# Kernel optimization log

Measured on AMD Instinct MI355X. Metric: run time of the kernel, lower is better.

The kernel has to match this reference:

```python
import jax, jax.numpy as jnp
import numpy as np

N = 50000      # nodes
E = 800000     # edges
GENE = 64      # gene_dim
HID = 128      # hidden_dim
NCLS = 10      # num_classes
EPS = 1e-5


def setup_inputs() -> dict:
    key = jax.random.key(0)
    ks = jax.random.split(key, 4)
    inp = {
        "x": jax.random.normal(ks[0], (N, GENE), jnp.float32),
        "edge_index": jax.random.randint(ks[1], (2, E), 0, N),
    }
    # PNA-style conv: concat([x, 4 aggregators x 3 scalers]) -> 13*d_in features
    dims = [(GENE, HID), (HID, 2 * HID), (2 * HID, HID), (HID, HID // 2)]
    for i, (din, dout) in enumerate(dims, 1):
        k = jax.random.fold_in(key, i)
        inp[f"W{i}"] = jax.random.normal(k, (13 * din, dout), jnp.float32) / float(np.sqrt(13 * din))
        inp[f"b{i}"] = jnp.zeros((dout,), jnp.float32)
        inp[f"gamma{i}"] = jnp.ones((dout,), jnp.float32)
        inp[f"beta{i}"] = jnp.zeros((dout,), jnp.float32)
    inp["Wc"] = jax.random.normal(ks[2], (HID // 2, NCLS), jnp.float32) / float(np.sqrt(HID // 2))
    inp["bc"] = jnp.zeros((NCLS,), jnp.float32)
    return inp


def _pna(x, src, dst, deg, log_deg, delta, W, b):
    # gather source features along edges: [E, d]
    msg = x[src]
    cnt = jnp.maximum(deg, 1.0)[:, None]
    s = jax.ops.segment_sum(msg, dst, num_segments=N)
    mean = s / cnt
    mean_sq = jax.ops.segment_sum(msg * msg, dst, num_segments=N) / cnt
    std = jnp.sqrt(jnp.maximum(mean_sq - mean * mean, 0.0) + EPS)
    has = (deg > 0)[:, None]
    mn = jnp.where(has, jax.ops.segment_min(msg, dst, num_segments=N), 0.0)
    mx = jnp.where(has, jax.ops.segment_max(msg, dst, num_segments=N), 0.0)
    aggs = jnp.concatenate([mean, mn, mx, std], axis=-1)  # [N, 4d]
    amp = (log_deg / delta)[:, None]                       # amplification scaler
    att = jnp.where(log_deg > 0, delta / jnp.maximum(log_deg, 1e-6), 1.0)[:, None]
    feat = jnp.concatenate([x, aggs, aggs * amp, aggs * att], axis=-1)  # [N, 13d]
    return feat @ W + b


def _bn(h, gamma, beta):
    m = h.mean(axis=0)
    v = h.var(axis=0)
    return (h - m) / jnp.sqrt(v + EPS) * gamma + beta


def reference(x, edge_index, W1, b1, gamma1, beta1, W2, b2, gamma2, beta2,
              W3, b3, gamma3, beta3, W4, b4, gamma4, beta4, Wc, bc):
    src, dst = edge_index[0], edge_index[1]
    deg = jax.ops.segment_sum(jnp.ones((E,), jnp.float32), dst, num_segments=N)
    log_deg = jnp.log1p(deg)
    delta = log_deg.mean()
    h = _pna(x, src, dst, deg, log_deg, delta, W1, b1)
    h = _bn(jax.nn.relu(h), gamma1, beta1)
    h = _pna(h, src, dst, deg, log_deg, delta, W2, b2)
    h = _bn(jax.nn.relu(h), gamma2, beta2)
    h = _pna(h, src, dst, deg, log_deg, delta, W3, b3)
    h = _bn(jax.nn.relu(h), gamma3, beta3)
    h = _pna(h, src, dst, deg, log_deg, delta, W4, b4)
    h = _bn(jax.nn.relu(h), gamma4, beta4)
    return h @ Wc + bc
```

## Files before the change

### kernel.cpp

```cpp
#include <hip/hip_runtime.h>
#include <hip/hip_bf16.h>

#define NN 50000
#define NE 800000
#define EPSV 1e-5f
#define NB 49

typedef _Float16 h8 __attribute__((ext_vector_type(8)));
typedef _Float16 h4 __attribute__((ext_vector_type(4)));
typedef float    f4 __attribute__((ext_vector_type(4)));


__global__ void k_deg(const int* __restrict__ dst, int* __restrict__ deg){
  int e = blockIdx.x*blockDim.x + threadIdx.x;
  if(e < NE) atomicAdd(&deg[dst[e]], 1);
}

__global__ void k_logdeg(const int* __restrict__ deg, float* __restrict__ logdeg,
                         float* __restrict__ dsum){
  int i = blockIdx.x*blockDim.x + threadIdx.x;
  float v = 0.f;
  if(i < NN){ v = log1pf((float)deg[i]); logdeg[i] = v; }
  __shared__ float sh[256];
  sh[threadIdx.x] = v; __syncthreads();
  for(int off=128; off>0; off>>=1){
    if(threadIdx.x < off) sh[threadIdx.x] += sh[threadIdx.x+off];
    __syncthreads();
  }
  if(threadIdx.x == 0) atomicAdd(dsum, sh[0]);
}

__global__ void k_scalers(const float* __restrict__ logdeg, const float* __restrict__ dsum,
                          float* __restrict__ amp, float* __restrict__ att){
  int i = blockIdx.x*blockDim.x + threadIdx.x;
  if(i >= NN) return;
  float delta = dsum[0] / (float)NN;
  float ld = logdeg[i];
  amp[i] = ld / delta;
  att[i] = (ld > 0.f) ? (delta / fmaxf(ld, 1e-6f)) : 1.f;
}

__global__ void k_scan1(const int* __restrict__ deg, int* __restrict__ rowptr,
                        int* __restrict__ bsum){
  __shared__ int buf[1024];
  int tid = threadIdx.x;
  int i = blockIdx.x*1024 + tid;
  int v = (i < NN) ? deg[i] : 0;
  buf[tid] = v; __syncthreads();
  for(int off=1; off<1024; off<<=1){
    int t = (tid >= off) ? buf[tid-off] : 0;
    __syncthreads();
    buf[tid] += t;
    __syncthreads();
  }
  if(i < NN) rowptr[i] = buf[tid] - v;
  if(tid == 1023) bsum[blockIdx.x] = buf[1023];
}

__global__ void k_scan2(int* __restrict__ bsum){
  if(threadIdx.x == 0){
    int s = 0;
    for(int b = 0; b < NB; b++){ int t = bsum[b]; bsum[b] = s; s += t; }
    bsum[NB] = s;
  }
}

__global__ void k_scan3(int* __restrict__ rowptr, int* __restrict__ cursor,
                        const int* __restrict__ bsum){
  int i = blockIdx.x*256 + threadIdx.x;
  if(i < NN){
    int v = rowptr[i] + bsum[i >> 10];
    rowptr[i] = v; cursor[i] = v;
  }
  if(i == NN) rowptr[NN] = bsum[NB];
}

__global__ void k_fill(const int* __restrict__ src, const int* __restrict__ dst,
                       int* __restrict__ cursor, int* __restrict__ colidx){
  int e = blockIdx.x*blockDim.x + threadIdx.x;
  if(e < NE){
    int pos = atomicAdd(&cursor[dst[e]], 1);
    colidx[pos] = src[e];
  }
}

__global__ void k_cvtx(const float* __restrict__ x, _Float16* __restrict__ act){
  int i = blockIdx.x*256 + threadIdx.x;
  if(i < NN*64) act[i] = (_Float16)x[i];
}

__global__ void k_coef_id(float* __restrict__ cs, float* __restrict__ csh,
                          _Float16* __restrict__ cs16, _Float16* __restrict__ csh16){
  int c = threadIdx.x;
  cs[c] = 1.f; csh[c] = 0.f;
  cs16[c] = (_Float16)1.f; csh16[c] = (_Float16)0.f;
}

__global__ void k_bn_coef(const float* __restrict__ colsum, const float* __restrict__ colss,
                          const float* __restrict__ gamma, const float* __restrict__ beta,
                          int dout, float* __restrict__ cs, float* __restrict__ csh,
                          _Float16* __restrict__ cs16, _Float16* __restrict__ csh16){
  int c = threadIdx.x;
  if(c >= dout) return;
  float mean = colsum[c] / (float)NN;
  float var  = colss[c] / (float)NN - mean*mean;
  float inv  = rsqrtf(fmaxf(var, 0.f) + EPSV);
  float a = inv * gamma[c];
  float b = beta[c] - mean * a;
  cs[c] = a; csh[c] = b;
  cs16[c] = (_Float16)a; csh16[c] = (_Float16)b;
}


__global__ __launch_bounds__(256) void k_agg8(
    const _Float16* __restrict__ act, int d,
    const int* __restrict__ rowptr, const int* __restrict__ colidx,
    const float* __restrict__ cs, const float* __restrict__ csh,
    _Float16* __restrict__ aggs, size_t aggN)
{
  int wv = threadIdx.x >> 6, lane = threadIdx.x & 63;
  int lpn = d >> 3;
  int npw = 64 / lpn;
  int n = blockIdx.x*(npw*4) + wv*npw + (lane / lpn);
  int c = (lane % lpn) * 8;
  if(n >= NN) return;
  int beg = rowptr[n], end = rowptr[n+1];
  const _Float16* hp = act + c;

  float s[8], q[8], mn[8], mx[8];
  #pragma unroll
  for(int j = 0; j < 8; j++){ s[j]=0.f; q[j]=0.f; mn[j]=INFINITY; mx[j]=-INFINITY; }

#define ACC8(v) { _Pragma("unroll") for(int j=0;j<8;j++){ float a=(float)(v)[j]; \
    s[j]+=a; q[j]+=a*a; mn[j]=fminf(mn[j],a); mx[j]=fmaxf(mx[j],a); } }

  int e = beg;
  for(; e+4 <= end; e+=4){
    int i0=colidx[e], i1=colidx[e+1], i2=colidx[e+2], i3=colidx[e+3];
    h8 v0 = *(const h8*)(hp + (size_t)i0*d);
    h8 v1 = *(const h8*)(hp + (size_t)i1*d);
    h8 v2 = *(const h8*)(hp + (size_t)i2*d);
    h8 v3 = *(const h8*)(hp + (size_t)i3*d);
    ACC8(v0) ACC8(v1) ACC8(v2) ACC8(v3)
  }
  for(; e < end; e++){
    h8 v = *(const h8*)(hp + (size_t)colidx[e]*d);
    ACC8(v)
  }
#undef ACC8

  float cnt = (end>beg) ? (float)(end-beg) : 1.f;
  h8 vm, vn, vx, vs;
  #pragma unroll
  for(int j = 0; j < 8; j++){
    float a = cs[c+j], b = csh[c+j];
    float mean_r = s[j]/cnt;
    float var_r  = fmaxf(q[j]/cnt - mean_r*mean_r, 0.f);
    float meanp = a*mean_r + b;
    float mnp = (a >= 0.f) ? a*mn[j]+b : a*mx[j]+b;
    float mxp = (a >= 0.f) ? a*mx[j]+b : a*mn[j]+b;
    float sdp = sqrtf(a*a*var_r + EPSV);
    if(end <= beg){ meanp = 0.f; mnp = 0.f; mxp = 0.f; sdp = sqrtf(EPSV); }
    vm[j] = (_Float16)meanp; vn[j] = (_Float16)mnp;
    vx[j] = (_Float16)mxp;   vs[j] = (_Float16)sdp;
  }

  _Float16* dst = aggs + (size_t)(c>>6)*aggN + (size_t)n*256 + (c & 63);
  *(h8*)(dst)       = vm;
  *(h8*)(dst + 64)  = vn;
  *(h8*)(dst + 128) = vx;
  *(h8*)(dst + 192) = vs;
}


struct PackJob { const float* W; _Float16* dst; int d, o, j0, start; };
struct PackArgs { PackJob job[9]; int total; };

__global__ void k_pack_all(PackArgs a){
  int idx = blockIdx.x*256 + threadIdx.x;
  if(idx >= a.total) return;
  int ji = 0;
  while(ji < 8 && idx >= a.job[ji+1].start) ji++;
  PackJob J = a.job[ji];
  int rel = idx - J.start;
  int j    = rel & 7;
  int lane = (rel >> 3) & 63;
  int rem  = rel >> 9;
  int ntiles = J.o >> 4;
  int kb = rem / ntiles;
  int nt = rem - kb*ntiles;
  int k = kb*32 + (lane>>4)*8 + j;
  int n = nt*16 + (lane&15);
  int srcrow;
  if(k < 64)       srcrow = J.j0 + k;
  else if(k < 320){ int t=k-64;  srcrow = (1+(t>>6))*J.d + J.j0 + (t&63); }
  else if(k < 576){ int t=k-320; srcrow = (5+(t>>6))*J.d + J.j0 + (t&63); }
  else            { int t=k-576; srcrow = (9+(t>>6))*J.d + J.j0 + (t&63); }
  J.dst[rel] = (_Float16)J.W[(size_t)srcrow*J.o + n];
}


__global__ __launch_bounds__(256) void k_mfma_fused(
    const _Float16* __restrict__ actIn, int d, int nch,
    const _Float16* __restrict__ aggs,
    const float* __restrict__ amp, const float* __restrict__ att,
    const _Float16* __restrict__ cs16, const _Float16* __restrict__ csh16,
    const _Float16* __restrict__ Wp, int o,
    const float* __restrict__ bias,
    _Float16* __restrict__ out)
{
  int tid  = threadIdx.x;
  int wv   = tid >> 6;
  int lane = tid & 63;
  int mi   = lane & 15;
  int q    = lane >> 4;
  int m0   = blockIdx.y * 128 + wv * 32;
  int c0   = blockIdx.x * 64;
  int ntiles = o >> 4;
  int nt0  = blockIdx.x * 4;

  int mrow[2];
  mrow[0] = min(m0 + mi,      NN-1);
  mrow[1] = min(m0 + 16 + mi, NN-1);
  _Float16 am16[2] = { (_Float16)amp[mrow[0]], (_Float16)amp[mrow[1]] };
  _Float16 at16[2] = { (_Float16)att[mrow[0]], (_Float16)att[mrow[1]] };
  const _Float16* hAb[2];
  const _Float16* agb[2];
  hAb[0] = actIn + (size_t)mrow[0]*d + q*8;
  hAb[1] = actIn + (size_t)mrow[1]*d + q*8;
  agb[0] = aggs + (size_t)mrow[0]*256 + q*8;
  agb[1] = aggs + (size_t)mrow[1]*256 + q*8;

  f4 acc[2][4] = {};
  const size_t aggN = (size_t)NN*256;

  for(int c = 0; c < nch; c++){
    const _Float16* Wpc = Wp + (size_t)c*832*o;
    auto bfrag = [&](int kb, int nn) -> h8 {
      return *(const h8*)(Wpc + (((size_t)kb*ntiles + nt0 + nn)*64 + lane)*8);
    };

    h8 ax[2][2];
    h8 ag[8][2];
    #pragma unroll
    for(int kb = 0; kb < 2; kb++){
      h8 sc = *(const h8*)(cs16  + c*64 + kb*32 + q*8);
      h8 sh = *(const h8*)(csh16 + c*64 + kb*32 + q*8);
      #pragma unroll
      for(int t = 0; t < 2; t++){
        h8 a = *(const h8*)(hAb[t] + c*64 + kb*32);
        ax[kb][t] = a*sc + sh;
      }
    }
    #pragma unroll
    for(int idx = 0; idx < 8; idx++)
      #pragma unroll
      for(int t = 0; t < 2; t++)
        ag[idx][t] = *(const h8*)(agb[t] + (size_t)c*aggN + idx*32);

    #pragma unroll
    for(int kb = 0; kb < 2; kb++)
      #pragma unroll
      for(int t = 0; t < 2; t++)
        #pragma unroll
        for(int nn = 0; nn < 4; nn++)
          acc[t][nn] = __builtin_amdgcn_mfma_f32_16x16x32_f16(ax[kb][t], bfrag(kb,nn), acc[t][nn], 0,0,0);

    #pragma unroll
    for(int idx = 0; idx < 8; idx++){
      #pragma unroll
      for(int t = 0; t < 2; t++){
        h8 apl = ag[idx][t];
        h8 aam = apl * am16[t];
        h8 aat = apl * at16[t];
        #pragma unroll
        for(int nn = 0; nn < 4; nn++){
          acc[t][nn] = __builtin_amdgcn_mfma_f32_16x16x32_f16(apl, bfrag(2+idx,  nn), acc[t][nn], 0,0,0);
          acc[t][nn] = __builtin_amdgcn_mfma_f32_16x16x32_f16(aam, bfrag(10+idx, nn), acc[t][nn], 0,0,0);
          acc[t][nn] = __builtin_amdgcn_mfma_f32_16x16x32_f16(aat, bfrag(18+idx, nn), acc[t][nn], 0,0,0);
        }
      }
    }
  }

  #pragma unroll
  for(int t = 0; t < 2; t++){
    #pragma unroll
    for(int nn = 0; nn < 4; nn++){
      int n = c0 + nn*16 + mi;
      float bv = bias[n];
      #pragma unroll
      for(int r = 0; r < 4; r++){
        int m = m0 + t*16 + q*4 + r;
        if(m < NN)
          out[(size_t)m*o + n] = (_Float16)fmaxf(bv + acc[t][nn][r], 0.f);
      }
    }
  }
}


__global__ __launch_bounds__(256) void k_bn_stats(const _Float16* __restrict__ H, int dout,
                                                  float* __restrict__ colsum, float* __restrict__ colss){
  int tid = threadIdx.x;
  int gid = blockIdx.x*256 + tid;
  int stride = gridDim.x*256;
  int total = NN * dout;
  float s = 0.f, ss = 0.f;
  for(int i = gid; i < total; i += stride){
    float v = (float)H[i];
    s += v; ss += v*v;
  }
  __shared__ float shs[256], shss[256];
  shs[tid] = s; shss[tid] = ss;
  __syncthreads();
  if(tid < dout){
    float ts = 0.f, tss = 0.f;
    for(int i = tid; i < 256; i += dout){ ts += shs[i]; tss += shss[i]; }
    atomicAdd(&colsum[tid], ts);
    atomicAdd(&colss[tid], tss);
  }
}


__global__ __launch_bounds__(256) void k_cls(const _Float16* __restrict__ h,
    const float* __restrict__ cs, const float* __restrict__ csh,
    const float* __restrict__ Wc, const float* __restrict__ bc,
    float* __restrict__ out){
  __shared__ float w[640];
  __shared__ float bb[16];
  __shared__ float sca[64], shb[64];
  int tid = threadIdx.x;
  for(int i = tid; i < 640; i += 256) w[i] = Wc[i];
  if(tid < 10) bb[tid] = bc[tid];
  if(tid < 64){ sca[tid] = cs[tid]; shb[tid] = csh[tid]; }
  __syncthreads();
  int idx = blockIdx.x*256 + tid;
  int n = idx >> 4;
  int c = idx & 15;
  if(n < NN && c < 10){
    float acc = bb[c];
    const _Float16* hp = h + (size_t)n*64;
    #pragma unroll
    for(int k = 0; k < 64; k++)
      acc += ((float)hp[k]*sca[k] + shb[k]) * w[k*10 + c];
    out[(size_t)n*10 + c] = acc;
  }
}


extern "C" void kernel_launch(void* const* d_in, const int* in_sizes, int n_in,
                              void* d_out, int out_size, void* d_ws, size_t ws_size,
                              hipStream_t stream){
  const float* x = (const float*)d_in[0];
  const int* edge = (const int*)d_in[1];
  const int* esrc = edge;
  const int* edst = edge + NE;
  const float* W[4]  = {(const float*)d_in[2],  (const float*)d_in[6],
                        (const float*)d_in[10], (const float*)d_in[14]};
  const float* bb[4] = {(const float*)d_in[3],  (const float*)d_in[7],
                        (const float*)d_in[11], (const float*)d_in[15]};
  const float* gm[4] = {(const float*)d_in[4],  (const float*)d_in[8],
                        (const float*)d_in[12], (const float*)d_in[16]};
  const float* bt[4] = {(const float*)d_in[5],  (const float*)d_in[9],
                        (const float*)d_in[13], (const float*)d_in[17]};
  const float* Wc = (const float*)d_in[18];
  const float* bc = (const float*)d_in[19];
  (void)in_sizes; (void)n_in; (void)out_size; (void)ws_size;

  char* p = (char*)d_ws;
  auto alloc = [&](size_t bytes)->char*{
    char* r = p; p += (bytes + 255) & ~(size_t)255; return r;
  };
  _Float16* act0 = (_Float16*)alloc((size_t)NN*256*2);
  _Float16* act1 = (_Float16*)alloc((size_t)NN*256*2);
  _Float16* aggs = (_Float16*)alloc((size_t)4*NN*256*2);
  int*   deg    = (int*)  alloc((size_t)NN*4);
  float* logdeg = (float*)alloc((size_t)NN*4);
  float* amp    = (float*)alloc((size_t)NN*4);
  float* att    = (float*)alloc((size_t)NN*4);
  int*   rowptr = (int*)  alloc((size_t)(NN+1)*4);
  int*   cursor = (int*)  alloc((size_t)NN*4);
  int*   colidx = (int*)  alloc((size_t)NE*4);
  int*   bsum   = (int*)  alloc((size_t)(NB+1)*4);
  float* colsumL= (float*)alloc(4*256*4);
  float* colssL = (float*)alloc(4*256*4);
  float* dsum   = (float*)alloc(256);
  float*    csA  = (float*)   alloc(256*4);
  float*    cshA = (float*)   alloc(256*4);
  float*    csB  = (float*)   alloc(256*4);
  float*    cshB = (float*)   alloc(256*4);
  _Float16* cs16A  = (_Float16*)alloc(256*2);
  _Float16* csh16A = (_Float16*)alloc(256*2);
  _Float16* cs16B  = (_Float16*)alloc(256*2);
  _Float16* csh16B = (_Float16*)alloc(256*2);

  const int din[4]  = {64, 128, 256, 128};
  const int dto[4]  = {128, 256, 128, 64};
  const size_t aggN = (size_t)NN*256;
  _Float16* WpL[4];
  PackArgs pa; int pj = 0, poff = 0;
  for(int l = 0; l < 4; l++){
    int nch = din[l]/64;
    WpL[l] = (_Float16*)alloc((size_t)nch*832*dto[l]*2);
    for(int c = 0; c < nch; c++){
      pa.job[pj] = { W[l], WpL[l] + (size_t)c*832*dto[l], din[l], dto[l], c*64, poff };
      poff += 832*dto[l]; pj++;
    }
  }
  pa.total = poff;

  hipMemsetAsync(deg, 0, (size_t)NN*4, stream);
  hipMemsetAsync(dsum, 0, 4, stream);
  hipMemsetAsync(colsumL, 0, 4*256*4, stream);
  hipMemsetAsync(colssL,  0, 4*256*4, stream);

  k_pack_all<<<(pa.total+255)/256, 256, 0, stream>>>(pa);
  k_deg     <<<(NE+255)/256, 256, 0, stream>>>(edst, deg);
  k_logdeg  <<<(NN+255)/256, 256, 0, stream>>>(deg, logdeg, dsum);
  k_scalers <<<(NN+255)/256, 256, 0, stream>>>(logdeg, dsum, amp, att);
  k_scan1   <<<NB, 1024, 0, stream>>>(deg, rowptr, bsum);
  k_scan2   <<<1, 64, 0, stream>>>(bsum);
  k_scan3   <<<(NN+256)/256, 256, 0, stream>>>(rowptr, cursor, bsum);
  k_fill    <<<(NE+255)/256, 256, 0, stream>>>(esrc, edst, cursor, colidx);
  k_cvtx    <<<(NN*64+255)/256, 256, 0, stream>>>(x, act0);
  k_coef_id <<<1, 256, 0, stream>>>(csA, cshA, cs16A, csh16A);

  _Float16* actIn = act0;  _Float16* actOut = act1;
  float *csI = csA, *cshI = cshA, *csO = csB, *cshO = cshB;
  _Float16 *cs16I = cs16A, *csh16I = csh16A, *cs16O = cs16B, *csh16O = csh16B;

  for(int l = 0; l < 4; l++){
    int d = din[l], o = dto[l];
    int nch = d / 64;
    int npb = (64 / (d >> 3)) * 4;
    k_agg8<<<(NN+npb-1)/npb, 256, 0, stream>>>(actIn, d, rowptr, colidx,
                                               csI, cshI, aggs, aggN);
    dim3 g(o/64, (NN+127)/128);
    k_mfma_fused<<<g, 256, 0, stream>>>(actIn, d, nch, aggs, amp, att,
                                        cs16I, csh16I, WpL[l], o, bb[l], actOut);
    k_bn_stats<<<256, 256, 0, stream>>>(actOut, o, colsumL + l*256, colssL + l*256);
    k_bn_coef<<<1, 256, 0, stream>>>(colsumL + l*256, colssL + l*256, gm[l], bt[l], o,
                                     csO, cshO, cs16O, csh16O);
    _Float16* ta = actIn; actIn = actOut; actOut = ta;
    float* tf;
    tf = csI;  csI = csO;  csO = tf;
    tf = cshI; cshI = cshO; cshO = tf;
    _Float16* th;
    th = cs16I;  cs16I = cs16O;  cs16O = th;
    th = csh16I; csh16I = csh16O; csh16O = th;
  }
  k_cls<<<(NN*16+255)/256, 256, 0, stream>>>(actIn, csI, cshI, Wc, bc, (float*)d_out);
}
```

Baseline: 804.4 us.

## Fuse BN column statistics into MFMA epilogue and unroll aggregation gather by 8

BatchNorm column sum and sum-of-squares are now accumulated in the GEMM epilogue through shared-memory atomics, followed by one global atomic per column per block. This removes the separate k_bn_stats kernel and its re-read of the activation output. The neighbour aggregation loop also gains an 8-wide unrolled gather so more loads are in flight. The cost is shared-memory atomic contention, more global atomics, and higher register pressure in the aggregation kernel. Statistics are computed from fp32 values before the fp16 store, so they can differ slightly from the old path.

```diff
diff --git a/kernel.cpp b/kernel.cpp
--- a/kernel.cpp
+++ b/kernel.cpp
@@ -7,7 +7,6 @@
 #define NB 49
 
 typedef _Float16 h8 __attribute__((ext_vector_type(8)));
-typedef _Float16 h4 __attribute__((ext_vector_type(4)));
 typedef float    f4 __attribute__((ext_vector_type(4)));
 
 
@@ -135,6 +134,19 @@
     s[j]+=a; q[j]+=a*a; mn[j]=fminf(mn[j],a); mx[j]=fmaxf(mx[j],a); } }
 
   int e = beg;
+  for(; e+8 <= end; e+=8){
+    int i0=colidx[e],   i1=colidx[e+1], i2=colidx[e+2], i3=colidx[e+3];
+    int i4=colidx[e+4], i5=colidx[e+5], i6=colidx[e+6], i7=colidx[e+7];
+    h8 v0 = *(const h8*)(hp + (size_t)i0*d);
+    h8 v1 = *(const h8*)(hp + (size_t)i1*d);
+    h8 v2 = *(const h8*)(hp + (size_t)i2*d);
+    h8 v3 = *(const h8*)(hp + (size_t)i3*d);
+    h8 v4 = *(const h8*)(hp + (size_t)i4*d);
+    h8 v5 = *(const h8*)(hp + (size_t)i5*d);
+    h8 v6 = *(const h8*)(hp + (size_t)i6*d);
+    h8 v7 = *(const h8*)(hp + (size_t)i7*d);
+    ACC8(v0) ACC8(v1) ACC8(v2) ACC8(v3) ACC8(v4) ACC8(v5) ACC8(v6) ACC8(v7)
+  }
   for(; e+4 <= end; e+=4){
     int i0=colidx[e], i1=colidx[e+1], i2=colidx[e+2], i3=colidx[e+3];
     h8 v0 = *(const h8*)(hp + (size_t)i0*d);
@@ -207,8 +219,10 @@
     const _Float16* __restrict__ cs16, const _Float16* __restrict__ csh16,
     const _Float16* __restrict__ Wp, int o,
     const float* __restrict__ bias,
-    _Float16* __restrict__ out)
+    _Float16* __restrict__ out,
+    float* __restrict__ colsum, float* __restrict__ colss)
 {
+  __shared__ float redS[64], redQ[64];
   int tid  = threadIdx.x;
   int wv   = tid >> 6;
   int lane = tid & 63;
@@ -218,6 +232,8 @@
   int c0   = blockIdx.x * 64;
   int ntiles = o >> 4;
   int nt0  = blockIdx.x * 4;
+
+  if(tid < 64){ redS[tid] = 0.f; redQ[tid] = 0.f; }
 
   int mrow[2];
   mrow[0] = min(m0 + mi,      NN-1);
@@ -283,42 +299,32 @@
     }
   }
 
+  __syncthreads();
+
   #pragma unroll
   for(int t = 0; t < 2; t++){
     #pragma unroll
     for(int nn = 0; nn < 4; nn++){
       int n = c0 + nn*16 + mi;
       float bv = bias[n];
+      float ps = 0.f, pq = 0.f;
       #pragma unroll
       for(int r = 0; r < 4; r++){
         int m = m0 + t*16 + q*4 + r;
-        if(m < NN)
-          out[(size_t)m*o + n] = (_Float16)fmaxf(bv + acc[t][nn][r], 0.f);
+        if(m < NN){
+          float v = fmaxf(bv + acc[t][nn][r], 0.f);
+          out[(size_t)m*o + n] = (_Float16)v;
+          ps += v; pq += v*v;
+        }
       }
+      atomicAdd(&redS[nn*16 + mi], ps);
+      atomicAdd(&redQ[nn*16 + mi], pq);
     }
   }
-}
-
-
-__global__ __launch_bounds__(256) void k_bn_stats(const _Float16* __restrict__ H, int dout,
-                                                  float* __restrict__ colsum, float* __restrict__ colss){
-  int tid = threadIdx.x;
-  int gid = blockIdx.x*256 + tid;
-  int stride = gridDim.x*256;
-  int total = NN * dout;
-  float s = 0.f, ss = 0.f;
-  for(int i = gid; i < total; i += stride){
-    float v = (float)H[i];
-    s += v; ss += v*v;
-  }
-  __shared__ float shs[256], shss[256];
-  shs[tid] = s; shss[tid] = ss;
   __syncthreads();
-  if(tid < dout){
-    float ts = 0.f, tss = 0.f;
-    for(int i = tid; i < 256; i += dout){ ts += shs[i]; tss += shss[i]; }
-    atomicAdd(&colsum[tid], ts);
-    atomicAdd(&colss[tid], tss);
+  if(tid < 64){
+    atomicAdd(&colsum[c0 + tid], redS[tid]);
+    atomicAdd(&colss[c0 + tid],  redQ[tid]);
   }
 }
 
@@ -438,8 +444,8 @@
                                                csI, cshI, aggs, aggN);
     dim3 g(o/64, (NN+127)/128);
     k_mfma_fused<<<g, 256, 0, stream>>>(actIn, d, nch, aggs, amp, att,
-                                        cs16I, csh16I, WpL[l], o, bb[l], actOut);
-    k_bn_stats<<<256, 256, 0, stream>>>(actOut, o, colsumL + l*256, colssL + l*256);
+                                        cs16I, csh16I, WpL[l], o, bb[l], actOut,
+                                        colsumL + l*256, colssL + l*256);
     k_bn_coef<<<1, 256, 0, stream>>>(colsumL + l*256, colssL + l*256, gm[l], bt[l], o,
                                      csO, cshO, cs16O, csh16O);
     _Float16* ta = actIn; actIn = actOut; actOut = ta;
```

New measurement: 743.6 us. 1.08x faster.
